# Performance work log

Hardware: AMD Instinct MI355X
Metric: run time of the kernel (lower is better)

## Reference

```python
import jax, jax.numpy as jnp
import numpy as np

B, V, F = 32, 1024, 16
A, P, NF = 32, 64, 128
C = P + A  # propagated feature width after concat with edge weights
D_OUT_IN = F + A + 2 * A * C  # 6192, input dim of output Dense


def setup_inputs() -> dict:
    key = jax.random.key(0)
    ks = jax.random.split(key, 4)
    return {
        "x": jax.random.normal(ks[0], (B, V, F), dtype=jnp.float32),
        "W_flr": jax.random.normal(ks[1], (F, P), dtype=jnp.float32) * (1.0 / np.sqrt(F)),
        "b_flr": jnp.zeros((P,), dtype=jnp.float32),
        "W_s": jax.random.normal(ks[2], (F, A), dtype=jnp.float32) * (1.0 / np.sqrt(F)),
        "b_s": jnp.zeros((A,), dtype=jnp.float32),
        "W_out": jax.random.normal(ks[3], (D_OUT_IN, NF), dtype=jnp.float32) * (1.0 / np.sqrt(D_OUT_IN)),
        "b_out": jnp.zeros((NF,), dtype=jnp.float32),
    }


def reference(x, W_flr, b_flr, W_s, b_s, W_out, b_out):
    # Per-vertex transforms
    feat = x @ W_flr + b_flr                      # (B,V,P)
    dist = x @ W_s + b_s                          # (B,V,A)
    ew = jnp.exp(-jnp.square(dist))               # (B,V,A) edge weights vertex->aggregator
    f = jnp.concatenate([feat, ew], axis=-1)      # (B,V,C)

    # Weighted broadcast then vertex-axis reduction (aggregator gather)
    w = jnp.transpose(ew, (0, 2, 1))              # (B,A,V)
    prod = w[..., None] * f[:, None, :, :]        # (B,A,V,C)
    agg_max = jnp.max(prod, axis=2)               # (B,A,C)
    agg_mean = jnp.mean(prod, axis=2)             # (B,A,C)
    agg = jnp.concatenate([agg_max, agg_mean], axis=-1)  # (B,A,2C)

    # Scatter aggregated features back to vertices, weighted by same edge weights
    upd = ew[..., None] * agg[:, None, :, :]      # (B,V,A,2C)
    upd = upd.reshape(B, V, A * 2 * C)            # (B,V,2AC)

    cat = jnp.concatenate([x, upd, ew], axis=-1)  # (B,V,F+2AC+A)
    return jnp.tanh(cat @ W_out + b_out)          # (B,V,NF)
```

## Files before the change

kernel.cpp:

```cpp
#include <hip/hip_runtime.h>
#include <hip/hip_bf16.h>
#include <math.h>

#define NB 32
#define NV 1024
#define NFT 16
#define NA 32
#define NP 64
#define NOUT 128
#define NC 96
#define NC2 192

#define NSPLIT 16
#define VPB 64

typedef __attribute__((ext_vector_type(8))) short bf16x8;
typedef __attribute__((ext_vector_type(4))) float f32x4;

__global__ __launch_bounds__(512, 2)
void k2p(const float* __restrict__ x,
         const float* __restrict__ W_flr,
         const float* __restrict__ b_flr,
         const float* __restrict__ W_s,
         const float* __restrict__ b_s,
         float* __restrict__ ewbuf,
         float* __restrict__ part) {
    __shared__ float xs[VPB][NFT];
    __shared__ float fs[VPB][NC];

    int b = blockIdx.x, vs = blockIdx.y, tid = threadIdx.x;
    int rowbase = b * NV + vs * VPB;

    if (tid < 256) {
        const float4* xsrc = (const float4*)(x + (size_t)rowbase * NFT);
        ((float4*)xs)[tid] = xsrc[tid];
    }
    __syncthreads();

    {
        int c  = tid & 127;
        int rh = tid >> 7;
        if (c < NC) {
            float Wcol[NFT], bias;
            if (c < NP) {
                bias = b_flr[c];
#pragma unroll
                for (int k = 0; k < NFT; ++k) Wcol[k] = W_flr[k * NP + c];
            } else {
                int a = c - NP;
                bias = b_s[a];
#pragma unroll
                for (int k = 0; k < NFT; ++k) Wcol[k] = W_s[k * NA + a];
            }
#pragma unroll
            for (int r0 = 0; r0 < 16; ++r0) {
                int r = rh * 16 + r0;
                float xr[NFT];
#pragma unroll
                for (int q = 0; q < 4; ++q)
                    ((float4*)xr)[q] = ((const float4*)xs[r])[q];
                float acc = bias;
#pragma unroll
                for (int k = 0; k < NFT; ++k)
                    acc = fmaf(xr[k], Wcol[k], acc);
                if (c >= NP) {
                    acc = __expf(-acc * acc);
                    ewbuf[(size_t)(rowbase + r) * NA + (c - NP)] = acc;
                }
                fs[r][c] = acc;
            }
        }
    }
    __syncthreads();

    int a  = tid >> 4;
    int c0 = (tid & 15) * 6;
    int ea = NP + a;

    float sm[6], mx[6];
#pragma unroll
    for (int j = 0; j < 6; ++j) { sm[j] = 0.f; mx[j] = -INFINITY; }

#pragma unroll 4
    for (int r = 0; r < VPB; ++r) {
        float e = fs[r][ea];
        float2 fA = *(const float2*)&fs[r][c0];
        float2 fB = *(const float2*)&fs[r][c0 + 2];
        float2 fC = *(const float2*)&fs[r][c0 + 4];
        float ff[6] = {fA.x, fA.y, fB.x, fB.y, fC.x, fC.y};
#pragma unroll
        for (int j = 0; j < 6; ++j) {
            float p = e * ff[j];
            sm[j] += p;
            mx[j] = fmaxf(mx[j], p);
        }
    }

    float* pb = part + (size_t)((b * NSPLIT + vs) * NA + a) * NC2;
#pragma unroll
    for (int q = 0; q < 3; ++q) {
        float2 vm = {mx[2 * q], mx[2 * q + 1]};
        float2 vsum = {sm[2 * q], sm[2 * q + 1]};
        *(float2*)&pb[c0 + 2 * q]      = vm;
        *(float2*)&pb[NC + c0 + 2 * q] = vsum;
    }
}

__global__ void k23(const float* __restrict__ part,
                    const float* __restrict__ W_out,
                    float* __restrict__ Gp) {
    __shared__ float aggL[NC2];
    int b = blockIdx.x, a = blockIdx.y, tid = threadIdx.x;

    {
        const float* pb = part + (size_t)(b * NSPLIT * NA + a) * NC2 + tid;
        const size_t stride = (size_t)NA * NC2;
        if (tid < NC) {
            float m = -INFINITY;
#pragma unroll
            for (int vsi = 0; vsi < NSPLIT; ++vsi)
                m = fmaxf(m, pb[vsi * stride]);
            aggL[tid] = m;
        } else {
            float s = 0.f;
#pragma unroll
            for (int vsi = 0; vsi < NSPLIT; ++vsi)
                s += pb[vsi * stride];
            aggL[tid] = s * (1.0f / (float)NV);
        }
    }
    __syncthreads();

    if (tid < NOUT) {
        int n = tid;
        const float* wr = W_out + (size_t)(NFT + a * NC2) * NOUT + n;
        float acc = W_out[(size_t)(NFT + NA * NC2 + a) * NOUT + n];
#pragma unroll 8
        for (int c = 0; c < NC2; ++c)
            acc = fmaf(aggL[c], wr[(size_t)c * NOUT], acc);
        Gp[(size_t)(b * NA + a) * NOUT + n] = acc;
    }
}

#define MB 64
#define SWZ(r, k)  (((r) << 6) + ((k) ^ (((r) & 7) << 3)))
#define SWZB(n, k) (((n) << 6) + ((k) ^ (((((n) >> 3) & 7) ^ ((n) & 7)) << 3)))

__device__ inline void f2hl(float v, ushort& h, ushort& l) {
    __hip_bfloat16 hb = __float2bfloat16(v);
    float hf = __bfloat162float(hb);
    __hip_bfloat16 lb = __float2bfloat16(v - hf);
    h = *(ushort*)&hb;
    l = *(ushort*)&lb;
}

__global__ void k4_mfma(const float* __restrict__ x,
                        const float* __restrict__ ewbuf,
                        const float* __restrict__ Gp,
                        const float* __restrict__ W_out,
                        const float* __restrict__ b_out,
                        float* __restrict__ out) {
    __shared__ ushort AsH[MB * 64], AsL[MB * 64];
    __shared__ ushort BsH[NOUT * 64], BsL[NOUT * 64];
    __shared__ float  bs[NOUT];

    int rb = blockIdx.x;
    int b  = blockIdx.y;
    int tid = threadIdx.x;
    int rowbase = b * NV + rb * MB;

    {
        float4 v = ((const float4*)(x + (size_t)rowbase * NFT))[tid];
        int r = tid >> 2, kq = (tid & 3) * 4;
        float vv[4] = {v.x, v.y, v.z, v.w};
        ushort h[4], l[4];
#pragma unroll
        for (int j = 0; j < 4; ++j) f2hl(vv[j], h[j], l[j]);
        *(uint*)&AsH[SWZ(r, kq)]     = (uint)h[0] | ((uint)h[1] << 16);
        *(uint*)&AsH[SWZ(r, kq + 2)] = (uint)h[2] | ((uint)h[3] << 16);
        *(uint*)&AsL[SWZ(r, kq)]     = (uint)l[0] | ((uint)l[1] << 16);
        *(uint*)&AsL[SWZ(r, kq + 2)] = (uint)l[2] | ((uint)l[3] << 16);
    }
    {
        const float4* es4 = (const float4*)(ewbuf + (size_t)rowbase * NA);
#pragma unroll
        for (int t = 0; t < 2; ++t) {
            int i = tid * 2 + t;
            float4 v = es4[i];
            int r = i >> 3, kq = 16 + (i & 7) * 4;
            float vv[4] = {v.x, v.y, v.z, v.w};
            ushort h[4], l[4];
#pragma unroll
            for (int j = 0; j < 4; ++j) f2hl(vv[j], h[j], l[j]);
            *(uint*)&AsH[SWZ(r, kq)]     = (uint)h[0] | ((uint)h[1] << 16);
            *(uint*)&AsH[SWZ(r, kq + 2)] = (uint)h[2] | ((uint)h[3] << 16);
            *(uint*)&AsL[SWZ(r, kq)]     = (uint)l[0] | ((uint)l[1] << 16);
            *(uint*)&AsL[SWZ(r, kq + 2)] = (uint)l[2] | ((uint)l[3] << 16);
        }
    }
    {
#pragma unroll
        for (int t = 0; t < 2; ++t) {
            int i = tid * 2 + t;
            int r = i >> 3, kq = 48 + (i & 7) * 2;
            *(uint*)&AsH[SWZ(r, kq)] = 0u;
            *(uint*)&AsL[SWZ(r, kq)] = 0u;
        }
    }
    {
#pragma unroll
        for (int t = 0; t < 2; ++t) {
            int i = tid * 2 + t;
            int k = i >> 5, nq = (i & 31) * 4;
            float4 v = ((const float4*)W_out)[i];
            float vv[4] = {v.x, v.y, v.z, v.w};
#pragma unroll
            for (int j = 0; j < 4; ++j) {
                ushort h, l;
                f2hl(vv[j], h, l);
                BsH[SWZB(nq + j, k)] = h;
                BsL[SWZB(nq + j, k)] = l;
            }
        }
    }
    {
        const float4* gp4 = (const float4*)(Gp + (size_t)b * NA * NOUT);
#pragma unroll
        for (int t = 0; t < 4; ++t) {
            int i = tid * 4 + t;
            int a = i >> 5, nq = (i & 31) * 4;
            float4 v = gp4[i];
            int k = 16 + a;
            float vv[4] = {v.x, v.y, v.z, v.w};
#pragma unroll
            for (int j = 0; j < 4; ++j) {
                ushort h, l;
                f2hl(vv[j], h, l);
                BsH[SWZB(nq + j, k)] = h;
                BsL[SWZB(nq + j, k)] = l;
            }
        }
    }
    {
#pragma unroll
        for (int t = 0; t < 4; ++t) {
            int i = tid * 4 + t;
            int n = i >> 3, kq = 48 + (i & 7) * 2;
            *(uint*)&BsH[SWZB(n, kq)] = 0u;
            *(uint*)&BsL[SWZB(n, kq)] = 0u;
        }
    }
    if (tid < NOUT) bs[tid] = b_out[tid];

    __syncthreads();

    int w = tid >> 6, lane = tid & 63;
    int r16 = lane & 15, kg = lane >> 4, k0 = kg * 8;
    int arow = w * 16 + r16;

    bf16x8 AH0 = *(const bf16x8*)&AsH[SWZ(arow, k0)];
    bf16x8 AH1 = *(const bf16x8*)&AsH[SWZ(arow, 32 + k0)];
    bf16x8 AL0 = *(const bf16x8*)&AsL[SWZ(arow, k0)];
    bf16x8 AL1 = *(const bf16x8*)&AsL[SWZ(arow, 32 + k0)];

    int orow0 = rowbase + w * 16 + kg * 4;

#pragma unroll
    for (int nt = 0; nt < 8; ++nt) {
        int n = nt * 16 + r16;
        bf16x8 BH0 = *(const bf16x8*)&BsH[SWZB(n, k0)];
        bf16x8 BH1 = *(const bf16x8*)&BsH[SWZB(n, 32 + k0)];
        bf16x8 BL0 = *(const bf16x8*)&BsL[SWZB(n, k0)];
        bf16x8 BL1 = *(const bf16x8*)&BsL[SWZB(n, 32 + k0)];
        float bias = bs[n];
        f32x4 acc = {bias, bias, bias, bias};
        acc = __builtin_amdgcn_mfma_f32_16x16x32_bf16(AH0, BH0, acc, 0, 0, 0);
        acc = __builtin_amdgcn_mfma_f32_16x16x32_bf16(AL0, BH0, acc, 0, 0, 0);
        acc = __builtin_amdgcn_mfma_f32_16x16x32_bf16(AH0, BL0, acc, 0, 0, 0);
        acc = __builtin_amdgcn_mfma_f32_16x16x32_bf16(AH1, BH1, acc, 0, 0, 0);
        acc = __builtin_amdgcn_mfma_f32_16x16x32_bf16(AL1, BH1, acc, 0, 0, 0);
        acc = __builtin_amdgcn_mfma_f32_16x16x32_bf16(AH1, BL1, acc, 0, 0, 0);
#pragma unroll
        for (int rg = 0; rg < 4; ++rg) {
            float s = acc[rg];
            s = fminf(fmaxf(s, -15.f), 15.f);
            float e = __expf(2.f * s);
            out[(size_t)(orow0 + rg) * NOUT + n] =
                (e - 1.f) * __builtin_amdgcn_rcpf(e + 1.f);
        }
    }
}

extern "C" void kernel_launch(void* const* d_in, const int* in_sizes, int n_in,
                              void* d_out, int out_size, void* d_ws, size_t ws_size,
                              hipStream_t stream) {
    const float* x     = (const float*)d_in[0];
    const float* W_flr = (const float*)d_in[1];
    const float* b_flr = (const float*)d_in[2];
    const float* W_s   = (const float*)d_in[3];
    const float* b_s   = (const float*)d_in[4];
    const float* W_out = (const float*)d_in[5];
    const float* b_out = (const float*)d_in[6];
    float* out = (float*)d_out;

    float* ewbuf = (float*)d_ws;
    float* part  = ewbuf + (size_t)NB * NV * NA;
    float* Gp    = part  + (size_t)NB * NSPLIT * NA * NC2;

    {
        dim3 g(NB, NSPLIT);
        k2p<<<g, 512, 0, stream>>>(x, W_flr, b_flr, W_s, b_s, ewbuf, part);
    }
    {
        dim3 g(NB, NA);
        k23<<<g, 192, 0, stream>>>(part, W_out, Gp);
    }
    {
        dim3 g(NV / MB, NB);
        k4_mfma<<<g, 256, 0, stream>>>(x, ewbuf, Gp, W_out, b_out, out);
    }
}
```

Baseline: 38.07 us.

## Fuse three kernels into one cooperative kernel with grid-wide syncs

```diff
diff --git a/kernel.cpp b/kernel.cpp
--- a/kernel.cpp
+++ b/kernel.cpp
@@ -1,6 +1,9 @@
 #include <hip/hip_runtime.h>
+#include <hip/hip_cooperative_groups.h>
 #include <hip/hip_bf16.h>
 #include <math.h>
+
+namespace cg = cooperative_groups;
 
 #define NB 32
 #define NV 1024
@@ -13,136 +16,11 @@
 
 #define NSPLIT 16
 #define VPB 64
+#define MB 64
 
 typedef __attribute__((ext_vector_type(8))) short bf16x8;
 typedef __attribute__((ext_vector_type(4))) float f32x4;
 
-__global__ __launch_bounds__(512, 2)
-void k2p(const float* __restrict__ x,
-         const float* __restrict__ W_flr,
-         const float* __restrict__ b_flr,
-         const float* __restrict__ W_s,
-         const float* __restrict__ b_s,
-         float* __restrict__ ewbuf,
-         float* __restrict__ part) {
-    __shared__ float xs[VPB][NFT];
-    __shared__ float fs[VPB][NC];
-
-    int b = blockIdx.x, vs = blockIdx.y, tid = threadIdx.x;
-    int rowbase = b * NV + vs * VPB;
-
-    if (tid < 256) {
-        const float4* xsrc = (const float4*)(x + (size_t)rowbase * NFT);
-        ((float4*)xs)[tid] = xsrc[tid];
-    }
-    __syncthreads();
-
-    {
-        int c  = tid & 127;
-        int rh = tid >> 7;
-        if (c < NC) {
-            float Wcol[NFT], bias;
-            if (c < NP) {
-                bias = b_flr[c];
-#pragma unroll
-                for (int k = 0; k < NFT; ++k) Wcol[k] = W_flr[k * NP + c];
-            } else {
-                int a = c - NP;
-                bias = b_s[a];
-#pragma unroll
-                for (int k = 0; k < NFT; ++k) Wcol[k] = W_s[k * NA + a];
-            }
-#pragma unroll
-            for (int r0 = 0; r0 < 16; ++r0) {
-                int r = rh * 16 + r0;
-                float xr[NFT];
-#pragma unroll
-                for (int q = 0; q < 4; ++q)
-                    ((float4*)xr)[q] = ((const float4*)xs[r])[q];
-                float acc = bias;
-#pragma unroll
-                for (int k = 0; k < NFT; ++k)
-                    acc = fmaf(xr[k], Wcol[k], acc);
-                if (c >= NP) {
-                    acc = __expf(-acc * acc);
-                    ewbuf[(size_t)(rowbase + r) * NA + (c - NP)] = acc;
-                }
-                fs[r][c] = acc;
-            }
-        }
-    }
-    __syncthreads();
-
-    int a  = tid >> 4;
-    int c0 = (tid & 15) * 6;
-    int ea = NP + a;
-
-    float sm[6], mx[6];
-#pragma unroll
-    for (int j = 0; j < 6; ++j) { sm[j] = 0.f; mx[j] = -INFINITY; }
-
-#pragma unroll 4
-    for (int r = 0; r < VPB; ++r) {
-        float e = fs[r][ea];
-        float2 fA = *(const float2*)&fs[r][c0];
-        float2 fB = *(const float2*)&fs[r][c0 + 2];
-        float2 fC = *(const float2*)&fs[r][c0 + 4];
-        float ff[6] = {fA.x, fA.y, fB.x, fB.y, fC.x, fC.y};
-#pragma unroll
-        for (int j = 0; j < 6; ++j) {
-            float p = e * ff[j];
-            sm[j] += p;
-            mx[j] = fmaxf(mx[j], p);
-        }
-    }
-
-    float* pb = part + (size_t)((b * NSPLIT + vs) * NA + a) * NC2;
-#pragma unroll
-    for (int q = 0; q < 3; ++q) {
-        float2 vm = {mx[2 * q], mx[2 * q + 1]};
-        float2 vsum = {sm[2 * q], sm[2 * q + 1]};
-        *(float2*)&pb[c0 + 2 * q]      = vm;
-        *(float2*)&pb[NC + c0 + 2 * q] = vsum;
-    }
-}
-
-__global__ void k23(const float* __restrict__ part,
-                    const float* __restrict__ W_out,
-                    float* __restrict__ Gp) {
-    __shared__ float aggL[NC2];
-    int b = blockIdx.x, a = blockIdx.y, tid = threadIdx.x;
-
-    {
-        const float* pb = part + (size_t)(b * NSPLIT * NA + a) * NC2 + tid;
-        const size_t stride = (size_t)NA * NC2;
-        if (tid < NC) {
-            float m = -INFINITY;
-#pragma unroll
-            for (int vsi = 0; vsi < NSPLIT; ++vsi)
-                m = fmaxf(m, pb[vsi * stride]);
-            aggL[tid] = m;
-        } else {
-            float s = 0.f;
-#pragma unroll
-            for (int vsi = 0; vsi < NSPLIT; ++vsi)
-                s += pb[vsi * stride];
-            aggL[tid] = s * (1.0f / (float)NV);
-        }
-    }
-    __syncthreads();
-
-    if (tid < NOUT) {
-        int n = tid;
-        const float* wr = W_out + (size_t)(NFT + a * NC2) * NOUT + n;
-        float acc = W_out[(size_t)(NFT + NA * NC2 + a) * NOUT + n];
-#pragma unroll 8
-        for (int c = 0; c < NC2; ++c)
-            acc = fmaf(aggL[c], wr[(size_t)c * NOUT], acc);
-        Gp[(size_t)(b * NA + a) * NOUT + n] = acc;
-    }
-}
-
-#define MB 64
 #define SWZ(r, k)  (((r) << 6) + ((k) ^ (((r) & 7) << 3)))
 #define SWZB(n, k) (((n) << 6) + ((k) ^ (((((n) >> 3) & 7) ^ ((n) & 7)) << 3)))
 
@@ -154,139 +32,284 @@
     l = *(ushort*)&lb;
 }
 
-__global__ void k4_mfma(const float* __restrict__ x,
-                        const float* __restrict__ ewbuf,
-                        const float* __restrict__ Gp,
-                        const float* __restrict__ W_out,
-                        const float* __restrict__ b_out,
-                        float* __restrict__ out) {
-    __shared__ ushort AsH[MB * 64], AsL[MB * 64];
-    __shared__ ushort BsH[NOUT * 64], BsL[NOUT * 64];
-    __shared__ float  bs[NOUT];
-
-    int rb = blockIdx.x;
-    int b  = blockIdx.y;
-    int tid = threadIdx.x;
-    int rowbase = b * NV + rb * MB;
+struct SmP1 { float xs[VPB][NFT]; float fs[VPB][NC]; };
+struct SmP2 { float aggL[4][NC2]; };
+struct SmP3 { ushort AsH[MB * 64]; ushort AsL[MB * 64];
+              ushort BsH[NOUT * 64]; ushort BsL[NOUT * 64]; float bs[NOUT]; };
+union SmemU { SmP1 p1; SmP2 p2; SmP3 p3; };
+
+__global__ __launch_bounds__(512, 2)
+void garnet_fused(const float* __restrict__ x,
+                  const float* __restrict__ W_flr,
+                  const float* __restrict__ b_flr,
+                  const float* __restrict__ W_s,
+                  const float* __restrict__ b_s,
+                  const float* __restrict__ W_out,
+                  const float* __restrict__ b_out,
+                  float* __restrict__ ewbuf,
+                  float* __restrict__ part,
+                  float* __restrict__ Gp,
+                  float* __restrict__ out) {
+    __shared__ SmemU S;
+    cg::grid_group grid = cg::this_grid();
+    int bid = blockIdx.x, tid = threadIdx.x;
+
+    for (int s = 0; s < 2; ++s) {
+        int slice = bid * 2 + s;
+        int b = slice >> 4, vs = slice & 15;
+        int rowbase = b * NV + vs * VPB;
+
+        if (tid < 256) {
+            const float4* xsrc = (const float4*)(x + (size_t)rowbase * NFT);
+            ((float4*)S.p1.xs)[tid] = xsrc[tid];
+        }
+        __syncthreads();
+
+        {
+            int c  = tid & 127;
+            int rh = tid >> 7;
+            if (c < NC) {
+                float Wcol[NFT], bias;
+                if (c < NP) {
+                    bias = b_flr[c];
+#pragma unroll
+                    for (int k = 0; k < NFT; ++k) Wcol[k] = W_flr[k * NP + c];
+                } else {
+                    int a = c - NP;
+                    bias = b_s[a];
+#pragma unroll
+                    for (int k = 0; k < NFT; ++k) Wcol[k] = W_s[k * NA + a];
+                }
+#pragma unroll
+                for (int r0 = 0; r0 < 16; ++r0) {
+                    int r = rh * 16 + r0;
+                    float xr[NFT];
+#pragma unroll
+                    for (int q = 0; q < 4; ++q)
+                        ((float4*)xr)[q] = ((const float4*)S.p1.xs[r])[q];
+                    float acc = bias;
+#pragma unroll
+                    for (int k = 0; k < NFT; ++k)
+                        acc = fmaf(xr[k], Wcol[k], acc);
+                    if (c >= NP) {
+                        acc = __expf(-acc * acc);
+                        ewbuf[(size_t)(rowbase + r) * NA + (c - NP)] = acc;
+                    }
+                    S.p1.fs[r][c] = acc;
+                }
+            }
+        }
+        __syncthreads();
+
+        int a  = tid >> 4;
+        int c0 = (tid & 15) * 6;
+        int ea = NP + a;
+
+        float sm[6], mx[6];
+#pragma unroll
+        for (int j = 0; j < 6; ++j) { sm[j] = 0.f; mx[j] = -INFINITY; }
+
+#pragma unroll 4
+        for (int r = 0; r < VPB; ++r) {
+            float e = S.p1.fs[r][ea];
+            float2 fA = *(const float2*)&S.p1.fs[r][c0];
+            float2 fB = *(const float2*)&S.p1.fs[r][c0 + 2];
+            float2 fC = *(const float2*)&S.p1.fs[r][c0 + 4];
+            float ff[6] = {fA.x, fA.y, fB.x, fB.y, fC.x, fC.y};
+#pragma unroll
+            for (int j = 0; j < 6; ++j) {
+                float p = e * ff[j];
+                sm[j] += p;
+                mx[j] = fmaxf(mx[j], p);
+            }
+        }
+
+        float* pb = part + (size_t)((b * NSPLIT + vs) * NA + a) * NC2;
+#pragma unroll
+        for (int q = 0; q < 3; ++q) {
+            float2 vm = {mx[2 * q], mx[2 * q + 1]};
+            float2 vsum = {sm[2 * q], sm[2 * q + 1]};
+            *(float2*)&pb[c0 + 2 * q]      = vm;
+            *(float2*)&pb[NC + c0 + 2 * q] = vsum;
+        }
+        __syncthreads();
+    }
+
+    grid.sync();
 
     {
-        float4 v = ((const float4*)(x + (size_t)rowbase * NFT))[tid];
-        int r = tid >> 2, kq = (tid & 3) * 4;
-        float vv[4] = {v.x, v.y, v.z, v.w};
-        ushort h[4], l[4];
-#pragma unroll
-        for (int j = 0; j < 4; ++j) f2hl(vv[j], h[j], l[j]);
-        *(uint*)&AsH[SWZ(r, kq)]     = (uint)h[0] | ((uint)h[1] << 16);
-        *(uint*)&AsH[SWZ(r, kq + 2)] = (uint)h[2] | ((uint)h[3] << 16);
-        *(uint*)&AsL[SWZ(r, kq)]     = (uint)l[0] | ((uint)l[1] << 16);
-        *(uint*)&AsL[SWZ(r, kq + 2)] = (uint)l[2] | ((uint)l[3] << 16);
+        int h = tid >> 7;
+        int t = tid & 127;
+        int unit = bid * 4 + h;
+        int b = unit >> 5, a = unit & 31;
+
+        const float* pb = part + (size_t)(b * NSPLIT * NA + a) * NC2;
+        const size_t stride = (size_t)NA * NC2;
+
+#pragma unroll
+        for (int cell = 0; cell < 2; ++cell) {
+            int j = t + cell * 128;
+            if (j < NC2) {
+                if (j < NC) {
+                    float m = -INFINITY;
+#pragma unroll
+                    for (int vsi = 0; vsi < NSPLIT; ++vsi)
+                        m = fmaxf(m, pb[vsi * stride + j]);
+                    S.p2.aggL[h][j] = m;
+                } else {
+                    float sv = 0.f;
+#pragma unroll
+                    for (int vsi = 0; vsi < NSPLIT; ++vsi)
+                        sv += pb[vsi * stride + j];
+                    S.p2.aggL[h][j] = sv * (1.0f / (float)NV);
+                }
+            }
+        }
+        __syncthreads();
+
+        {
+            int n = t;
+            const float* wr = W_out + (size_t)(NFT + a * NC2) * NOUT + n;
+            float acc = W_out[(size_t)(NFT + NA * NC2 + a) * NOUT + n];
+#pragma unroll 8
+            for (int c = 0; c < NC2; ++c)
+                acc = fmaf(S.p2.aggL[h][c], wr[(size_t)c * NOUT], acc);
+            Gp[(size_t)(b * NA + a) * NOUT + n] = acc;
+        }
     }
+
+    grid.sync();
+
     {
-        const float4* es4 = (const float4*)(ewbuf + (size_t)rowbase * NA);
-#pragma unroll
-        for (int t = 0; t < 2; ++t) {
-            int i = tid * 2 + t;
-            float4 v = es4[i];
-            int r = i >> 3, kq = 16 + (i & 7) * 4;
-            float vv[4] = {v.x, v.y, v.z, v.w};
-            ushort h[4], l[4];
-#pragma unroll
-            for (int j = 0; j < 4; ++j) f2hl(vv[j], h[j], l[j]);
-            *(uint*)&AsH[SWZ(r, kq)]     = (uint)h[0] | ((uint)h[1] << 16);
-            *(uint*)&AsH[SWZ(r, kq + 2)] = (uint)h[2] | ((uint)h[3] << 16);
-            *(uint*)&AsL[SWZ(r, kq)]     = (uint)l[0] | ((uint)l[1] << 16);
-            *(uint*)&AsL[SWZ(r, kq + 2)] = (uint)l[2] | ((uint)l[3] << 16);
-        }
-    }
-    {
-#pragma unroll
-        for (int t = 0; t < 2; ++t) {
-            int i = tid * 2 + t;
-            int r = i >> 3, kq = 48 + (i & 7) * 2;
-            *(uint*)&AsH[SWZ(r, kq)] = 0u;
-            *(uint*)&AsL[SWZ(r, kq)] = 0u;
-        }
-    }
-    {
-#pragma unroll
-        for (int t = 0; t < 2; ++t) {
-            int i = tid * 2 + t;
-            int k = i >> 5, nq = (i & 31) * 4;
-            float4 v = ((const float4*)W_out)[i];
-            float vv[4] = {v.x, v.y, v.z, v.w};
+        int b = bid & 31;
+
+        if (tid < 256) {
+#pragma unroll
+            for (int t = 0; t < 2; ++t) {
+                int i = tid * 2 + t;
+                int k = i >> 5, nq = (i & 31) * 4;
+                float4 v = ((const float4*)W_out)[i];
+                float vv[4] = {v.x, v.y, v.z, v.w};
+#pragma unroll
+                for (int j = 0; j < 4; ++j) {
+                    ushort h, l;
+                    f2hl(vv[j], h, l);
+                    S.p3.BsH[SWZB(nq + j, k)] = h;
+                    S.p3.BsL[SWZB(nq + j, k)] = l;
+                }
+            }
+            const float4* gp4 = (const float4*)(Gp + (size_t)b * NA * NOUT);
+#pragma unroll
+            for (int t = 0; t < 4; ++t) {
+                int i = tid * 4 + t;
+                int a = i >> 5, nq = (i & 31) * 4;
+                float4 v = gp4[i];
+                int k = 16 + a;
+                float vv[4] = {v.x, v.y, v.z, v.w};
+#pragma unroll
+                for (int j = 0; j < 4; ++j) {
+                    ushort h, l;
+                    f2hl(vv[j], h, l);
+                    S.p3.BsH[SWZB(nq + j, k)] = h;
+                    S.p3.BsL[SWZB(nq + j, k)] = l;
+                }
+            }
+#pragma unroll
+            for (int t = 0; t < 4; ++t) {
+                int i = tid * 4 + t;
+                int n = i >> 3, kq = 48 + (i & 7) * 2;
+                *(uint*)&S.p3.BsH[SWZB(n, kq)] = 0u;
+                *(uint*)&S.p3.BsL[SWZB(n, kq)] = 0u;
+            }
+        }
+        if (tid < NOUT) S.p3.bs[tid] = b_out[tid];
+
+        for (int s = 0; s < 2; ++s) {
+            int tile = s * 256 + bid;
+            int rb = tile >> 5;
+            int rowbase = b * NV + rb * MB;
+
+            if (s) __syncthreads();
+
+            if (tid < 256) {
+                {
+                    float4 v = ((const float4*)(x + (size_t)rowbase * NFT))[tid];
+                    int r = tid >> 2, kq = (tid & 3) * 4;
+                    float vv[4] = {v.x, v.y, v.z, v.w};
+                    ushort h[4], l[4];
+#pragma unroll
+                    for (int j = 0; j < 4; ++j) f2hl(vv[j], h[j], l[j]);
+                    *(uint*)&S.p3.AsH[SWZ(r, kq)]     = (uint)h[0] | ((uint)h[1] << 16);
+                    *(uint*)&S.p3.AsH[SWZ(r, kq + 2)] = (uint)h[2] | ((uint)h[3] << 16);
+                    *(uint*)&S.p3.AsL[SWZ(r, kq)]     = (uint)l[0] | ((uint)l[1] << 16);
+                    *(uint*)&S.p3.AsL[SWZ(r, kq + 2)] = (uint)l[2] | ((uint)l[3] << 16);
+                }
+                {
+                    const float4* es4 = (const float4*)(ewbuf + (size_t)rowbase * NA);
+#pragma unroll
+                    for (int t = 0; t < 2; ++t) {
+                        int i = tid * 2 + t;
+                        float4 v = es4[i];
+                        int r = i >> 3, kq = 16 + (i & 7) * 4;
+                        float vv[4] = {v.x, v.y, v.z, v.w};
+                        ushort h[4], l[4];
+#pragma unroll
+                        for (int j = 0; j < 4; ++j) f2hl(vv[j], h[j], l[j]);
+                        *(uint*)&S.p3.AsH[SWZ(r, kq)]     = (uint)h[0] | ((uint)h[1] << 16);
+                        *(uint*)&S.p3.AsH[SWZ(r, kq + 2)] = (uint)h[2] | ((uint)h[3] << 16);
+                        *(uint*)&S.p3.AsL[SWZ(r, kq)]     = (uint)l[0] | ((uint)l[1] << 16);
+                        *(uint*)&S.p3.AsL[SWZ(r, kq + 2)] = (uint)l[2] | ((uint)l[3] << 16);
+                    }
+                }
+                {
+#pragma unroll
+                    for (int t = 0; t < 2; ++t) {
+                        int i = tid * 2 + t;
+                        int r = i >> 3, kq = 48 + (i & 7) * 2;
+                        *(uint*)&S.p3.AsH[SWZ(r, kq)] = 0u;
+                        *(uint*)&S.p3.AsL[SWZ(r, kq)] = 0u;
+                    }
+                }
+            }
+            __syncthreads();
+
+            int w8 = tid >> 6, lane = tid & 63;
+            int rgrp = w8 & 3, nh = w8 >> 2;
+            int r16 = lane & 15, kg = lane >> 4, k0 = kg * 8;
+            int arow = rgrp * 16 + r16;
+
+            bf16x8 AH0 = *(const bf16x8*)&S.p3.AsH[SWZ(arow, k0)];
+            bf16x8 AH1 = *(const bf16x8*)&S.p3.AsH[SWZ(arow, 32 + k0)];
+            bf16x8 AL0 = *(const bf16x8*)&S.p3.AsL[SWZ(arow, k0)];
+            bf16x8 AL1 = *(const bf16x8*)&S.p3.AsL[SWZ(arow, 32 + k0)];
+
+            int orow0 = rowbase + rgrp * 16 + kg * 4;
+
 #pragma unroll
             for (int j = 0; j < 4; ++j) {
-                ushort h, l;
-                f2hl(vv[j], h, l);
-                BsH[SWZB(nq + j, k)] = h;
-                BsL[SWZB(nq + j, k)] = l;
-            }
-        }
-    }
-    {
-        const float4* gp4 = (const float4*)(Gp + (size_t)b * NA * NOUT);
-#pragma unroll
-        for (int t = 0; t < 4; ++t) {
-            int i = tid * 4 + t;
-            int a = i >> 5, nq = (i & 31) * 4;
-            float4 v = gp4[i];
-            int k = 16 + a;
-            float vv[4] = {v.x, v.y, v.z, v.w};
-#pragma unroll
-            for (int j = 0; j < 4; ++j) {
-                ushort h, l;
-                f2hl(vv[j], h, l);
-                BsH[SWZB(nq + j, k)] = h;
-                BsL[SWZB(nq + j, k)] = l;
-            }
-        }
-    }
-    {
-#pragma unroll
-        for (int t = 0; t < 4; ++t) {
-            int i = tid * 4 + t;
-            int n = i >> 3, kq = 48 + (i & 7) * 2;
-            *(uint*)&BsH[SWZB(n, kq)] = 0u;
-            *(uint*)&BsL[SWZB(n, kq)] = 0u;
-        }
-    }
-    if (tid < NOUT) bs[tid] = b_out[tid];
-
-    __syncthreads();
-
-    int w = tid >> 6, lane = tid & 63;
-    int r16 = lane & 15, kg = lane >> 4, k0 = kg * 8;
-    int arow = w * 16 + r16;
-
-    bf16x8 AH0 = *(const bf16x8*)&AsH[SWZ(arow, k0)];
-    bf16x8 AH1 = *(const bf16x8*)&AsH[SWZ(arow, 32 + k0)];
-    bf16x8 AL0 = *(const bf16x8*)&AsL[SWZ(arow, k0)];
-    bf16x8 AL1 = *(const bf16x8*)&AsL[SWZ(arow, 32 + k0)];
-
-    int orow0 = rowbase + w * 16 + kg * 4;
-
-#pragma unroll
-    for (int nt = 0; nt < 8; ++nt) {
-        int n = nt * 16 + r16;
-        bf16x8 BH0 = *(const bf16x8*)&BsH[SWZB(n, k0)];
-        bf16x8 BH1 = *(const bf16x8*)&BsH[SWZB(n, 32 + k0)];
-        bf16x8 BL0 = *(const bf16x8*)&BsL[SWZB(n, k0)];
-        bf16x8 BL1 = *(const bf16x8*)&BsL[SWZB(n, 32 + k0)];
-        float bias = bs[n];
-        f32x4 acc = {bias, bias, bias, bias};
-        acc = __builtin_amdgcn_mfma_f32_16x16x32_bf16(AH0, BH0, acc, 0, 0, 0);
-        acc = __builtin_amdgcn_mfma_f32_16x16x32_bf16(AL0, BH0, acc, 0, 0, 0);
-        acc = __builtin_amdgcn_mfma_f32_16x16x32_bf16(AH0, BL0, acc, 0, 0, 0);
-        acc = __builtin_amdgcn_mfma_f32_16x16x32_bf16(AH1, BH1, acc, 0, 0, 0);
-        acc = __builtin_amdgcn_mfma_f32_16x16x32_bf16(AL1, BH1, acc, 0, 0, 0);
-        acc = __builtin_amdgcn_mfma_f32_16x16x32_bf16(AH1, BL1, acc, 0, 0, 0);
-#pragma unroll
-        for (int rg = 0; rg < 4; ++rg) {
-            float s = acc[rg];
-            s = fminf(fmaxf(s, -15.f), 15.f);
-            float e = __expf(2.f * s);
-            out[(size_t)(orow0 + rg) * NOUT + n] =
-                (e - 1.f) * __builtin_amdgcn_rcpf(e + 1.f);
+                int nt = nh * 4 + j;
+                int n = nt * 16 + r16;
+                bf16x8 BH0 = *(const bf16x8*)&S.p3.BsH[SWZB(n, k0)];
+                bf16x8 BH1 = *(const bf16x8*)&S.p3.BsH[SWZB(n, 32 + k0)];
+                bf16x8 BL0 = *(const bf16x8*)&S.p3.BsL[SWZB(n, k0)];
+                bf16x8 BL1 = *(const bf16x8*)&S.p3.BsL[SWZB(n, 32 + k0)];
+                float bias = S.p3.bs[n];
+                f32x4 acc = {bias, bias, bias, bias};
+                acc = __builtin_amdgcn_mfma_f32_16x16x32_bf16(AH0, BH0, acc, 0, 0, 0);
+                acc = __builtin_amdgcn_mfma_f32_16x16x32_bf16(AL0, BH0, acc, 0, 0, 0);
+                acc = __builtin_amdgcn_mfma_f32_16x16x32_bf16(AH0, BL0, acc, 0, 0, 0);
+                acc = __builtin_amdgcn_mfma_f32_16x16x32_bf16(AH1, BH1, acc, 0, 0, 0);
+                acc = __builtin_amdgcn_mfma_f32_16x16x32_bf16(AL1, BH1, acc, 0, 0, 0);
+                acc = __builtin_amdgcn_mfma_f32_16x16x32_bf16(AH1, BL1, acc, 0, 0, 0);
+#pragma unroll
+                for (int rg = 0; rg < 4; ++rg) {
+                    float sv = acc[rg];
+                    sv = fminf(fmaxf(sv, -15.f), 15.f);
+                    float e = __expf(2.f * sv);
+                    out[(size_t)(orow0 + rg) * NOUT + n] =
+                        (e - 1.f) * __builtin_amdgcn_rcpf(e + 1.f);
+                }
+            }
         }
     }
 }
@@ -307,16 +330,12 @@
     float* part  = ewbuf + (size_t)NB * NV * NA;
     float* Gp    = part  + (size_t)NB * NSPLIT * NA * NC2;
 
-    {
-        dim3 g(NB, NSPLIT);
-        k2p<<<g, 512, 0, stream>>>(x, W_flr, b_flr, W_s, b_s, ewbuf, part);
-    }
-    {
-        dim3 g(NB, NA);
-        k23<<<g, 192, 0, stream>>>(part, W_out, Gp);
-    }
-    {
-        dim3 g(NV / MB, NB);
-        k4_mfma<<<g, 256, 0, stream>>>(x, ewbuf, Gp, W_out, b_out, out);
-    }
+    void* kargs[] = {
+        (void*)&x, (void*)&W_flr, (void*)&b_flr, (void*)&W_s, (void*)&b_s,
+        (void*)&W_out, (void*)&b_out, (void*)&ewbuf, (void*)&part,
+        (void*)&Gp, (void*)&out
+    };
+    hipLaunchCooperativeKernel((void*)garnet_fused,
+                               dim3(256), dim3(512),
+                               kargs, 0, stream);
 }
```

Measured after the change: 113.7 us. +198.7%, slower.

## Register-tile aggregator reduction in k2p and pair batches per k23 block

Applied to the files above, without the earlier changes.

```diff
diff --git a/kernel.cpp b/kernel.cpp
--- a/kernel.cpp
+++ b/kernel.cpp
@@ -25,8 +25,10 @@
          const float* __restrict__ b_s,
          float* __restrict__ ewbuf,
          float* __restrict__ part) {
-    __shared__ float xs[VPB][NFT];
-    __shared__ float fs[VPB][NC];
+    __shared__ float SM[7168];
+    float (*xs)[NFT] = (float (*)[NFT])SM;
+    float (*fs)[NC]  = (float (*)[NC])(SM + 1024);
+    float* comb = SM;
 
     int b = blockIdx.x, vs = blockIdx.y, tid = threadIdx.x;
     int rowbase = b * NV + vs * VPB;
@@ -73,71 +75,118 @@
     }
     __syncthreads();
 
-    int a  = tid >> 4;
-    int c0 = (tid & 15) * 6;
-    int ea = NP + a;
-
-    float sm[6], mx[6];
-#pragma unroll
-    for (int j = 0; j < 6; ++j) { sm[j] = 0.f; mx[j] = -INFINITY; }
+    int rsplit = tid >> 8;
+    int u  = tid & 255;
+    int a0 = (u >> 5) * 4;
+    int c0 = (u & 31) * 3;
+    int rb = rsplit * 32;
+
+    float sm[4][3], mx[4][3];
+#pragma unroll
+    for (int i = 0; i < 4; ++i)
+#pragma unroll
+        for (int j = 0; j < 3; ++j) { sm[i][j] = 0.f; mx[i][j] = -INFINITY; }
 
 #pragma unroll 4
-    for (int r = 0; r < VPB; ++r) {
-        float e = fs[r][ea];
-        float2 fA = *(const float2*)&fs[r][c0];
-        float2 fB = *(const float2*)&fs[r][c0 + 2];
-        float2 fC = *(const float2*)&fs[r][c0 + 4];
-        float ff[6] = {fA.x, fA.y, fB.x, fB.y, fC.x, fC.y};
-#pragma unroll
-        for (int j = 0; j < 6; ++j) {
-            float p = e * ff[j];
-            sm[j] += p;
-            mx[j] = fmaxf(mx[j], p);
-        }
-    }
-
-    float* pb = part + (size_t)((b * NSPLIT + vs) * NA + a) * NC2;
-#pragma unroll
-    for (int q = 0; q < 3; ++q) {
-        float2 vm = {mx[2 * q], mx[2 * q + 1]};
-        float2 vsum = {sm[2 * q], sm[2 * q + 1]};
-        *(float2*)&pb[c0 + 2 * q]      = vm;
-        *(float2*)&pb[NC + c0 + 2 * q] = vsum;
+    for (int r0 = 0; r0 < 32; ++r0) {
+        int r = rb + r0;
+        float4 e4 = *(const float4*)&fs[r][NP + a0];
+        float2 f2 = *(const float2*)&fs[r][c0];
+        float f1 = fs[r][c0 + 2];
+        float ff[3] = {f2.x, f2.y, f1};
+        float ee[4] = {e4.x, e4.y, e4.z, e4.w};
+#pragma unroll
+        for (int i = 0; i < 4; ++i)
+#pragma unroll
+            for (int j = 0; j < 3; ++j) {
+                float p = ee[i] * ff[j];
+                sm[i][j] += p;
+                mx[i][j] = fmaxf(mx[i][j], p);
+            }
+    }
+
+    __syncthreads();
+
+    if (rsplit == 0) {
+        float* cb = comb + u * 26;
+#pragma unroll
+        for (int i = 0; i < 4; ++i) {
+            float2 v0 = {sm[i][0], sm[i][1]};
+            float2 v1 = {sm[i][2], mx[i][0]};
+            float2 v2 = {mx[i][1], mx[i][2]};
+            *(float2*)&cb[i * 6]     = v0;
+            *(float2*)&cb[i * 6 + 2] = v1;
+            *(float2*)&cb[i * 6 + 4] = v2;
+        }
+    }
+    __syncthreads();
+    if (rsplit == 1) {
+        const float* cb = comb + u * 26;
+        float* pb = part + (size_t)((b * NSPLIT + vs) * NA) * NC2;
+#pragma unroll
+        for (int i = 0; i < 4; ++i) {
+            float2 v0 = *(const float2*)&cb[i * 6];
+            float2 v1 = *(const float2*)&cb[i * 6 + 2];
+            float2 v2 = *(const float2*)&cb[i * 6 + 4];
+            float osm0 = v0.x, osm1 = v0.y, osm2 = v1.x;
+            float omx0 = v1.y, omx1 = v2.x, omx2 = v2.y;
+            int a = a0 + i;
+            float m0 = fmaxf(mx[i][0], omx0);
+            float m1 = fmaxf(mx[i][1], omx1);
+            float m2 = fmaxf(mx[i][2], omx2);
+            float s0 = sm[i][0] + osm0;
+            float s1 = sm[i][1] + osm1;
+            float s2 = sm[i][2] + osm2;
+            float2 wm = {m0, m1};
+            float2 ws = {s0, s1};
+            *(float2*)&pb[a * NC2 + c0] = wm;
+            pb[a * NC2 + c0 + 2] = m2;
+            *(float2*)&pb[a * NC2 + NC + c0] = ws;
+            pb[a * NC2 + NC + c0 + 2] = s2;
+        }
     }
 }
 
 __global__ void k23(const float* __restrict__ part,
                     const float* __restrict__ W_out,
                     float* __restrict__ Gp) {
-    __shared__ float aggL[NC2];
-    int b = blockIdx.x, a = blockIdx.y, tid = threadIdx.x;
-
-    {
-        const float* pb = part + (size_t)(b * NSPLIT * NA + a) * NC2 + tid;
-        const size_t stride = (size_t)NA * NC2;
-        if (tid < NC) {
-            float m = -INFINITY;
-#pragma unroll
-            for (int vsi = 0; vsi < NSPLIT; ++vsi)
-                m = fmaxf(m, pb[vsi * stride]);
-            aggL[tid] = m;
-        } else {
-            float s = 0.f;
-#pragma unroll
-            for (int vsi = 0; vsi < NSPLIT; ++vsi)
-                s += pb[vsi * stride];
-            aggL[tid] = s * (1.0f / (float)NV);
-        }
-    }
-    __syncthreads();
-
-    if (tid < NOUT) {
-        int n = tid;
+    __shared__ float aggL[2][NC2];
+    int bq = blockIdx.x, a = blockIdx.y, tid = threadIdx.x;
+    int h = tid >> 7;
+    int t = tid & 127;
+    int b = bq * 2 + h;
+
+    const float* pb = part + (size_t)(b * NSPLIT * NA + a) * NC2;
+    const size_t stride = (size_t)NA * NC2;
+
+#pragma unroll
+    for (int cell = 0; cell < 2; ++cell) {
+        int j = t + cell * 128;
+        if (j < NC2) {
+            if (j < NC) {
+                float m = -INFINITY;
+#pragma unroll
+                for (int vsi = 0; vsi < NSPLIT; ++vsi)
+                    m = fmaxf(m, pb[vsi * stride + j]);
+                aggL[h][j] = m;
+            } else {
+                float s = 0.f;
+#pragma unroll
+                for (int vsi = 0; vsi < NSPLIT; ++vsi)
+                    s += pb[vsi * stride + j];
+                aggL[h][j] = s * (1.0f / (float)NV);
+            }
+        }
+    }
+    __syncthreads();
+
+    {
+        int n = t;
         const float* wr = W_out + (size_t)(NFT + a * NC2) * NOUT + n;
         float acc = W_out[(size_t)(NFT + NA * NC2 + a) * NOUT + n];
 #pragma unroll 8
         for (int c = 0; c < NC2; ++c)
-            acc = fmaf(aggL[c], wr[(size_t)c * NOUT], acc);
+            acc = fmaf(aggL[h][c], wr[(size_t)c * NOUT], acc);
         Gp[(size_t)(b * NA + a) * NOUT + n] = acc;
     }
 }
@@ -312,8 +361,8 @@
         k2p<<<g, 512, 0, stream>>>(x, W_flr, b_flr, W_s, b_s, ewbuf, part);
     }
     {
-        dim3 g(NB, NA);
-        k23<<<g, 192, 0, stream>>>(part, W_out, Gp);
+        dim3 g(NB / 2, NA);
+        k23<<<g, 256, 0, stream>>>(part, W_out, Gp);
     }
     {
         dim3 g(NV / MB, NB);
```

New measurement: 47.42 us. +24.6%, slower.

## Load A operands directly into registers and pre-pack B fragments in LDS

Applied to the files above, without the earlier changes.

```diff
diff --git a/kernel.cpp b/kernel.cpp
--- a/kernel.cpp
+++ b/kernel.cpp
@@ -143,8 +143,6 @@
 }
 
 #define MB 64
-#define SWZ(r, k)  (((r) << 6) + ((k) ^ (((r) & 7) << 3)))
-#define SWZB(n, k) (((n) << 6) + ((k) ^ (((((n) >> 3) & 7) ^ ((n) & 7)) << 3)))
 
 __device__ inline void f2hl(float v, ushort& h, ushort& l) {
     __hip_bfloat16 hb = __float2bfloat16(v);
@@ -160,8 +158,8 @@
                         const float* __restrict__ W_out,
                         const float* __restrict__ b_out,
                         float* __restrict__ out) {
-    __shared__ ushort AsH[MB * 64], AsL[MB * 64];
-    __shared__ ushort BsH[NOUT * 64], BsL[NOUT * 64];
+    __shared__ ushort BsH[1024 * 8];
+    __shared__ ushort BsL[1024 * 8];
     __shared__ float  bs[NOUT];
 
     int rb = blockIdx.x;
@@ -169,109 +167,68 @@
     int tid = threadIdx.x;
     int rowbase = b * NV + rb * MB;
 
-    {
-        float4 v = ((const float4*)(x + (size_t)rowbase * NFT))[tid];
-        int r = tid >> 2, kq = (tid & 3) * 4;
-        float vv[4] = {v.x, v.y, v.z, v.w};
-        ushort h[4], l[4];
-#pragma unroll
-        for (int j = 0; j < 4; ++j) f2hl(vv[j], h[j], l[j]);
-        *(uint*)&AsH[SWZ(r, kq)]     = (uint)h[0] | ((uint)h[1] << 16);
-        *(uint*)&AsH[SWZ(r, kq + 2)] = (uint)h[2] | ((uint)h[3] << 16);
-        *(uint*)&AsL[SWZ(r, kq)]     = (uint)l[0] | ((uint)l[1] << 16);
-        *(uint*)&AsL[SWZ(r, kq + 2)] = (uint)l[2] | ((uint)l[3] << 16);
-    }
-    {
-        const float4* es4 = (const float4*)(ewbuf + (size_t)rowbase * NA);
-#pragma unroll
-        for (int t = 0; t < 2; ++t) {
-            int i = tid * 2 + t;
-            float4 v = es4[i];
-            int r = i >> 3, kq = 16 + (i & 7) * 4;
-            float vv[4] = {v.x, v.y, v.z, v.w};
-            ushort h[4], l[4];
-#pragma unroll
-            for (int j = 0; j < 4; ++j) f2hl(vv[j], h[j], l[j]);
-            *(uint*)&AsH[SWZ(r, kq)]     = (uint)h[0] | ((uint)h[1] << 16);
-            *(uint*)&AsH[SWZ(r, kq + 2)] = (uint)h[2] | ((uint)h[3] << 16);
-            *(uint*)&AsL[SWZ(r, kq)]     = (uint)l[0] | ((uint)l[1] << 16);
-            *(uint*)&AsL[SWZ(r, kq + 2)] = (uint)l[2] | ((uint)l[3] << 16);
-        }
-    }
-    {
-#pragma unroll
-        for (int t = 0; t < 2; ++t) {
-            int i = tid * 2 + t;
-            int r = i >> 3, kq = 48 + (i & 7) * 2;
-            *(uint*)&AsH[SWZ(r, kq)] = 0u;
-            *(uint*)&AsL[SWZ(r, kq)] = 0u;
-        }
-    }
-    {
-#pragma unroll
-        for (int t = 0; t < 2; ++t) {
-            int i = tid * 2 + t;
-            int k = i >> 5, nq = (i & 31) * 4;
-            float4 v = ((const float4*)W_out)[i];
-            float vv[4] = {v.x, v.y, v.z, v.w};
-#pragma unroll
-            for (int j = 0; j < 4; ++j) {
-                ushort h, l;
-                f2hl(vv[j], h, l);
-                BsH[SWZB(nq + j, k)] = h;
-                BsL[SWZB(nq + j, k)] = l;
-            }
-        }
-    }
-    {
-        const float4* gp4 = (const float4*)(Gp + (size_t)b * NA * NOUT);
-#pragma unroll
-        for (int t = 0; t < 4; ++t) {
-            int i = tid * 4 + t;
-            int a = i >> 5, nq = (i & 31) * 4;
-            float4 v = gp4[i];
-            int k = 16 + a;
-            float vv[4] = {v.x, v.y, v.z, v.w};
-#pragma unroll
-            for (int j = 0; j < 4; ++j) {
-                ushort h, l;
-                f2hl(vv[j], h, l);
-                BsH[SWZB(nq + j, k)] = h;
-                BsL[SWZB(nq + j, k)] = l;
-            }
-        }
-    }
-    {
-#pragma unroll
-        for (int t = 0; t < 4; ++t) {
-            int i = tid * 4 + t;
-            int n = i >> 3, kq = 48 + (i & 7) * 2;
-            *(uint*)&BsH[SWZB(n, kq)] = 0u;
-            *(uint*)&BsL[SWZB(n, kq)] = 0u;
-        }
+#pragma unroll
+    for (int it = 0; it < 4; ++it) {
+        int u = it * 256 + tid;
+        int n = u & 127, koct = u >> 7;
+        float v[8];
+        if (koct < 2) {
+#pragma unroll
+            for (int j = 0; j < 8; ++j)
+                v[j] = W_out[(size_t)(koct * 8 + j) * NOUT + n];
+        } else if (koct < 6) {
+#pragma unroll
+            for (int j = 0; j < 8; ++j)
+                v[j] = Gp[(size_t)b * NA * NOUT + (size_t)(koct * 8 + j - 16) * NOUT + n];
+        } else {
+#pragma unroll
+            for (int j = 0; j < 8; ++j) v[j] = 0.f;
+        }
+        ushort h[8], l[8];
+#pragma unroll
+        for (int j = 0; j < 8; ++j) f2hl(v[j], h[j], l[j]);
+        int cidx = ((koct >> 2) * 512) + ((n >> 4) * 64) + ((koct & 3) * 16) + (n & 15);
+        *(bf16x8*)&BsH[cidx * 8] = *(bf16x8*)h;
+        *(bf16x8*)&BsL[cidx * 8] = *(bf16x8*)l;
     }
     if (tid < NOUT) bs[tid] = b_out[tid];
 
-    __syncthreads();
-
     int w = tid >> 6, lane = tid & 63;
-    int r16 = lane & 15, kg = lane >> 4, k0 = kg * 8;
+    int r16 = lane & 15, kg = lane >> 4;
     int arow = w * 16 + r16;
-
-    bf16x8 AH0 = *(const bf16x8*)&AsH[SWZ(arow, k0)];
-    bf16x8 AH1 = *(const bf16x8*)&AsH[SWZ(arow, 32 + k0)];
-    bf16x8 AL0 = *(const bf16x8*)&AsL[SWZ(arow, k0)];
-    bf16x8 AL1 = *(const bf16x8*)&AsL[SWZ(arow, 32 + k0)];
+    int grow = rowbase + arow;
+
+    float a0[8], a1[8];
+    if (kg < 2) {
+        *(float4*)&a0[0] = *(const float4*)&x[(size_t)grow * NFT + kg * 8];
+        *(float4*)&a0[4] = *(const float4*)&x[(size_t)grow * NFT + kg * 8 + 4];
+        *(float4*)&a1[0] = *(const float4*)&ewbuf[(size_t)grow * NA + 16 + kg * 8];
+        *(float4*)&a1[4] = *(const float4*)&ewbuf[(size_t)grow * NA + 16 + kg * 8 + 4];
+    } else {
+        *(float4*)&a0[0] = *(const float4*)&ewbuf[(size_t)grow * NA + (kg - 2) * 8];
+        *(float4*)&a0[4] = *(const float4*)&ewbuf[(size_t)grow * NA + (kg - 2) * 8 + 4];
+#pragma unroll
+        for (int j = 0; j < 8; ++j) a1[j] = 0.f;
+    }
+    ushort ah0[8], al0[8], ah1[8], al1[8];
+#pragma unroll
+    for (int j = 0; j < 8; ++j) f2hl(a0[j], ah0[j], al0[j]);
+#pragma unroll
+    for (int j = 0; j < 8; ++j) f2hl(a1[j], ah1[j], al1[j]);
+    bf16x8 AH0 = *(bf16x8*)ah0, AL0 = *(bf16x8*)al0;
+    bf16x8 AH1 = *(bf16x8*)ah1, AL1 = *(bf16x8*)al1;
+
+    __syncthreads();
 
     int orow0 = rowbase + w * 16 + kg * 4;
 
 #pragma unroll
     for (int nt = 0; nt < 8; ++nt) {
         int n = nt * 16 + r16;
-        bf16x8 BH0 = *(const bf16x8*)&BsH[SWZB(n, k0)];
-        bf16x8 BH1 = *(const bf16x8*)&BsH[SWZB(n, 32 + k0)];
-        bf16x8 BL0 = *(const bf16x8*)&BsL[SWZB(n, k0)];
-        bf16x8 BL1 = *(const bf16x8*)&BsL[SWZB(n, 32 + k0)];
+        bf16x8 BH0 = *(const bf16x8*)&BsH[(nt * 64 + lane) * 8];
+        bf16x8 BH1 = *(const bf16x8*)&BsH[(512 + nt * 64 + lane) * 8];
+        bf16x8 BL0 = *(const bf16x8*)&BsL[(nt * 64 + lane) * 8];
+        bf16x8 BL1 = *(const bf16x8*)&BsL[(512 + nt * 64 + lane) * 8];
         float bias = bs[n];
         f32x4 acc = {bias, bias, bias, bias};
         acc = __builtin_amdgcn_mfma_f32_16x16x32_bf16(AH0, BH0, acc, 0, 0, 0);
```

After: 39.10 us. +2.7%, slower.
